# Optimization experiments

Hardware: AMD Instinct MI355X
Metric: run time of the kernel (lower is better)

The kernel has to match this reference:

```python
import jax, jax.numpy as jnp
import numpy as np

N_TAYLOR = 4

def taylor_exp_poly(x, n_terms):
    # sum_{p=0}^{n_terms-1} x^p / p!  via Horner: 1 + x*(1 + x/2*(1 + x/3*(...)))
    acc = jnp.ones_like(x)
    for p in range(n_terms - 1, 0, -1):
        acc = 1.0 + (x / p) * acc
    return acc

def setup_inputs() -> dict:
    key = jax.random.key(0)
    kq, kk, kv = jax.random.split(key, 3)
    B, H, T, d_key, d_val = 4, 8, 2048, 32, 64
    Q = jax.random.normal(kq, (B, H, T, d_key), dtype=jnp.float32)
    K = jax.random.normal(kk, (B, H, T, d_key), dtype=jnp.float32)
    V = jax.random.normal(kv, (B, H, T, d_val), dtype=jnp.float32)
    return {"Q": Q, "K": K, "V": V}

def reference(Q, K, V):
    # Symmetry-aware Taylor-approximated attention (Heinsen & Kozachkov).
    # The tightly-packed degree-p feature maps phi_p satisfy
    #   phi_p(q) . phi_p(k) == (q.k / sqrt(d_key))^p / p!
    # so summing S/Z over all n_taylor terms equals attention with kernel
    #   w(q,k) = sum_{p<n_taylor} (q.k/sqrt(d_key))^p / p!   (truncated exp),
    # causally masked and normalized by the row-sum Z.
    d_key = Q.shape[-1]
    scale = 1.0 / jnp.sqrt(jnp.asarray(d_key, dtype=Q.dtype))
    scores = jnp.einsum('bhqd,bhkd->bhqk', Q, K) * scale  # [B,H,T,T]
    A = taylor_exp_poly(scores, N_TAYLOR)
    T = Q.shape[-2]
    causal = jnp.tril(jnp.ones((T, T), dtype=bool))  # [T,T]
    A = jnp.where(causal, A, jnp.zeros((), dtype=A.dtype))
    Z = jnp.sum(A, axis=-1, keepdims=True)           # [B,H,T,1]
    S = jnp.einsum('bhqk,bhkd->bhqd', A, V)          # [B,H,T,d_val]
    return S / Z
```

## Files before the change

kernel.cpp:

```cpp
#include <hip/hip_runtime.h>
#include <hip/hip_bf16.h>


typedef __attribute__((ext_vector_type(8))) short bf16x8;
typedef __attribute__((ext_vector_type(4))) float f32x4;
typedef __attribute__((ext_vector_type(16))) float f32x16;
typedef unsigned int u32;
typedef unsigned short u16;

namespace {

constexpr int T_SEQ = 2048;
constexpr int DK    = 32;
constexpr int DV    = 64;
constexpr int NBH   = 32;

constexpr float C1 = 0.17677669529663687f;
constexpr float C2 = 0.015625f;
constexpr float C3 = 9.2071195e-4f;

constexpr size_t KHI_OFF  = 0;
constexpr size_t KLO_OFF  = (size_t)NBH * T_SEQ * DK * 2;
constexpr size_t VTHI_OFF = KLO_OFF * 2;
constexpr size_t WS_NEED  = VTHI_OFF + (size_t)NBH * DV * T_SEQ * 2;

__device__ __forceinline__ u32 pack_hi2(float f0, float f1) {
  return (__float_as_uint(f0) >> 16) | (__float_as_uint(f1) & 0xffff0000u);
}
__device__ __forceinline__ float trunc_bf(float f) {
  return __uint_as_float(__float_as_uint(f) & 0xffff0000u);
}
__device__ __forceinline__ u16 bfhi(float f) { return (u16)(__float_as_uint(f) >> 16); }

__device__ __forceinline__ u32 pack_rn2(float f0, float f1) {
  union { __hip_bfloat16 h; u16 u; } a, b;
  a.h = __hip_bfloat16(f0);
  b.h = __hip_bfloat16(f1);
  return (u32)a.u | ((u32)b.u << 16);
}

__device__ __forceinline__ void permswap(u32& a, u32& b) {
  asm volatile("v_permlane32_swap_b32 %0, %1" : "+v"(a), "+v"(b));
}


__global__ void pack_kv(const float* __restrict__ Kg, const float* __restrict__ Vg,
                        u16* __restrict__ Khi, u16* __restrict__ Klo,
                        u16* __restrict__ Vthi) {
  __shared__ float tile[DV][33];
  const int bid = blockIdx.x;
  const int t   = threadIdx.x;
  if (bid < 2048) {
    size_t i = ((size_t)bid * 256 + t) * 4;
    float4 f = *(const float4*)(Kg + i);
    ushort4 h, l;
    h.x = bfhi(f.x); h.y = bfhi(f.y); h.z = bfhi(f.z); h.w = bfhi(f.w);
    l.x = bfhi(f.x - trunc_bf(f.x)); l.y = bfhi(f.y - trunc_bf(f.y));
    l.z = bfhi(f.z - trunc_bf(f.z)); l.w = bfhi(f.w - trunc_bf(f.w));
    *(ushort4*)(Khi + i) = h;
    *(ushort4*)(Klo + i) = l;
  } else {
    const int vb = bid - 2048;
    const int bh = vb >> 6;
    const int k0 = (vb & 63) * 32;
    {
      const int kl = t >> 3, c0 = (t & 7) * 8;
      const float* src = Vg + ((size_t)bh * T_SEQ + k0 + kl) * DV + c0;
      float4 a = *(const float4*)src;
      float4 b = *(const float4*)(src + 4);
      tile[c0 + 0][kl] = a.x; tile[c0 + 1][kl] = a.y;
      tile[c0 + 2][kl] = a.z; tile[c0 + 3][kl] = a.w;
      tile[c0 + 4][kl] = b.x; tile[c0 + 5][kl] = b.y;
      tile[c0 + 6][kl] = b.z; tile[c0 + 7][kl] = b.w;
    }
    __syncthreads();
    {
      const int cl = t >> 2, k8 = (t & 3) * 8;
      u32 h[4];
#pragma unroll
      for (int j = 0; j < 4; ++j)
        h[j] = pack_rn2(tile[cl][k8 + 2 * j], tile[cl][k8 + 2 * j + 1]);
      size_t off = ((size_t)(bh * DV + cl)) * T_SEQ + k0 + k8;
      *(uint4*)(Vthi + off) = make_uint4(h[0], h[1], h[2], h[3]);
    }
  }
}


__global__ __launch_bounds__(256, 4)
void taylor_attn_v6(const float* __restrict__ Qg, const u16* __restrict__ Khi,
                    const u16* __restrict__ Klo, const u16* __restrict__ Vthi,
                    float* __restrict__ Outg) {
  __shared__ __align__(16) float Sp[4 * 2048];
  __shared__ float Zp[4 * 32];

  const int tid = threadIdx.x;
  const int l   = tid & 63;
  const int w   = tid >> 6;
  const int cq  = l & 31;
  const int hi  = l >> 5;

  const int bid = blockIdx.x;
  const int xcd = bid & 7;
  const int r_  = bid >> 3;
  const int bh  = xcd * 4 + (r_ & 3);
  const int p   = r_ >> 2;

  const u16* kbh_hi = Khi + (size_t)bh * T_SEQ * DK;
  const u16* kbh_lo = Klo + (size_t)bh * T_SEQ * DK;
  const u16* vbh_hi = Vthi + (size_t)bh * DV * T_SEQ;
  const float* qb   = Qg + (size_t)bh * T_SEQ * DK;

#pragma unroll 1
  for (int ph = 0; ph < 2; ++ph) {
    const int s  = ph ? (63 - p) : p;
    const int q0 = s * 32;

    if (ph) __syncthreads();

    bf16x8 qfh[2], qfl[2];
#pragma unroll
    for (int t = 0; t < 2; ++t) {
      const float* qp = qb + (size_t)(q0 + cq) * DK + t * 16 + hi * 8;
      float4 a = *(const float4*)qp;
      float4 b = *(const float4*)(qp + 4);
      union { bf16x8 v; u32 u[4]; } H, L;
      H.u[0] = pack_hi2(a.x, a.y); H.u[1] = pack_hi2(a.z, a.w);
      H.u[2] = pack_hi2(b.x, b.y); H.u[3] = pack_hi2(b.z, b.w);
      L.u[0] = pack_hi2(a.x - trunc_bf(a.x), a.y - trunc_bf(a.y));
      L.u[1] = pack_hi2(a.z - trunc_bf(a.z), a.w - trunc_bf(a.w));
      L.u[2] = pack_hi2(b.x - trunc_bf(b.x), b.y - trunc_bf(b.y));
      L.u[3] = pack_hi2(b.z - trunc_bf(b.z), b.w - trunc_bf(b.w));
      qfh[t] = H.v; qfl[t] = L.v;
    }

    f32x16 acc[2];
#pragma unroll
    for (int ct = 0; ct < 2; ++ct)
#pragma unroll
      for (int r = 0; r < 16; ++r) acc[ct][r] = 0.f;
    float zacc = 0.f;

    for (int kt = w; kt <= s; kt += 4) {
      const int k0 = kt * 32;

      bf16x8 kfh[2], kfl[2];
#pragma unroll
      for (int t = 0; t < 2; ++t) {
        size_t off = (size_t)(k0 + cq) * DK + t * 16 + hi * 8;
        kfh[t] = *(const bf16x8*)(kbh_hi + off);
        kfl[t] = *(const bf16x8*)(kbh_lo + off);
      }
      bf16x8 vfr[4];
#pragma unroll
      for (int ct = 0; ct < 2; ++ct)
#pragma unroll
        for (int t = 0; t < 2; ++t)
          vfr[ct * 2 + t] = *(const bf16x8*)(
              vbh_hi + (size_t)(ct * 32 + cq) * T_SEQ + k0 + t * 16 + hi * 8);

      f32x16 d0, d1;
#pragma unroll
      for (int r = 0; r < 16; ++r) { d0[r] = 0.f; d1[r] = 0.f; }
      d0 = __builtin_amdgcn_mfma_f32_32x32x16_bf16(kfh[0], qfh[0], d0, 0, 0, 0);
      d1 = __builtin_amdgcn_mfma_f32_32x32x16_bf16(kfh[1], qfh[1], d1, 0, 0, 0);
      d0 = __builtin_amdgcn_mfma_f32_32x32x16_bf16(kfh[0], qfl[0], d0, 0, 0, 0);
      d1 = __builtin_amdgcn_mfma_f32_32x32x16_bf16(kfh[1], qfl[1], d1, 0, 0, 0);
      d0 = __builtin_amdgcn_mfma_f32_32x32x16_bf16(kfl[0], qfh[0], d0, 0, 0, 0);
      d1 = __builtin_amdgcn_mfma_f32_32x32x16_bf16(kfl[1], qfh[1], d1, 0, 0, 0);

      float wv[16];
      const bool diag = (kt == s);
#pragma unroll
      for (int r = 0; r < 16; ++r) {
        float sc = d0[r] + d1[r];
        float t_ = __builtin_fmaf(sc, C3, C2);
        t_       = __builtin_fmaf(sc, t_, C1);
        float wr = __builtin_fmaf(sc, t_, 1.0f);
        if (diag) {
          const int krel = (r & 3) + 8 * (r >> 2) + 4 * hi;
          wr = (krel <= cq) ? wr : 0.f;
        }
        zacc += wr;
        wv[r] = wr;
      }

      union { bf16x8 v; u32 u[4]; } WH[2];
#pragma unroll
      for (int t = 0; t < 2; ++t) {
        const int b = t * 8;
        u32 p0 = pack_rn2(wv[b + 0], wv[b + 1]);
        u32 p1 = pack_rn2(wv[b + 2], wv[b + 3]);
        u32 p2 = pack_rn2(wv[b + 4], wv[b + 5]);
        u32 p3 = pack_rn2(wv[b + 6], wv[b + 7]);
        permswap(p0, p2); permswap(p1, p3);
        WH[t].u[0] = p0; WH[t].u[1] = p1; WH[t].u[2] = p2; WH[t].u[3] = p3;
      }

#pragma unroll
      for (int ct = 0; ct < 2; ++ct)
#pragma unroll
        for (int t = 0; t < 2; ++t)
          acc[ct] = __builtin_amdgcn_mfma_f32_32x32x16_bf16(WH[t].v, vfr[ct * 2 + t],
                                                            acc[ct], 0, 0, 0);
    }

    {
      float zt = zacc + __shfl_xor(zacc, 32);
      if (hi == 0) Zp[w * 32 + cq] = zt;
    }
#pragma unroll
    for (int ct = 0; ct < 2; ++ct)
#pragma unroll
      for (int r = 0; r < 16; ++r) {
        const int qr = (r & 3) + 8 * (r >> 2) + 4 * hi;
        Sp[w * 2048 + qr * 64 + ct * 32 + cq] = acc[ct][r];
      }
    __syncthreads();

    const f32x4* S4 = (const f32x4*)Sp;
#pragma unroll
    for (int i = 0; i < 2; ++i) {
      const int e4  = tid + i * 256;
      const int row = e4 >> 4;
      f32x4 ssum = S4[e4] + S4[512 + e4] + S4[1024 + e4] + S4[1536 + e4];
      float z = Zp[row] + Zp[32 + row] + Zp[64 + row] + Zp[96 + row];
      float inv = 1.0f / z;
      float4 o;
      o.x = ssum[0] * inv; o.y = ssum[1] * inv;
      o.z = ssum[2] * inv; o.w = ssum[3] * inv;
      *(float4*)(Outg + ((size_t)bh * T_SEQ + q0 + row) * DV + (e4 & 15) * 4) = o;
    }
  }
}


constexpr int QT_FB = 64;
constexpr int KT_FB = 32;
constexpr int LDSW  = 40;
constexpr float SCALE = 0.17677669529663687f;

__global__ __launch_bounds__(256, 4)
void taylor_attn_fb(const float* __restrict__ Qg, const float* __restrict__ Kg,
                    const float* __restrict__ Vg, float* __restrict__ Outg) {
  __shared__ __align__(16) unsigned short Qhi[QT_FB * LDSW], Qlo[QT_FB * LDSW];
  __shared__ __align__(16) unsigned short Khi_[KT_FB * LDSW], Klo_[KT_FB * LDSW];
  __shared__ __align__(16) unsigned short Vthi_[DV * LDSW], Vtlo_[DV * LDSW];
  __shared__ __align__(16) unsigned Wp[4][16 * 32];

  const int tid  = threadIdx.x;
  const int lane = tid & 63;
  const int wid  = tid >> 6;
  const int m    = lane & 15;
  const int g    = lane >> 4;

  const int bid = blockIdx.x;
  const int v   = bid >> 3;
  const int bh  = (bid & 7) * 4 + (v >> 5);
  const int qt  = 31 - (v & 31);
  const int q0  = qt * QT_FB;

  const float* Qbase = Qg + ((size_t)bh * T_SEQ + q0) * DK;
  const float* Kbase = Kg + (size_t)bh * T_SEQ * DK;
  const float* Vbase = Vg + (size_t)bh * T_SEQ * DV;

#pragma unroll
  for (int p = 0; p < 2; ++p) {
    int e = tid + p * 256, row = e >> 3, c4 = (e & 7) * 4;
    float4 f = *(const float4*)(Qbase + row * DK + c4);
    uint2 h, l;
    h.x = pack_hi2(f.x, f.y); h.y = pack_hi2(f.z, f.w);
    l.x = pack_hi2(f.x - trunc_bf(f.x), f.y - trunc_bf(f.y));
    l.y = pack_hi2(f.z - trunc_bf(f.z), f.w - trunc_bf(f.w));
    *(uint2*)&Qhi[row * LDSW + c4] = h;
    *(uint2*)&Qlo[row * LDSW + c4] = l;
  }
  __syncthreads();

  const int wq = wid * 16;
  const bf16x8 qhi = *(const bf16x8*)&Qhi[(wq + m) * LDSW + g * 8];
  const bf16x8 qlo = *(const bf16x8*)&Qlo[(wq + m) * LDSW + g * 8];

  f32x4 acc[4];
#pragma unroll
  for (int ct = 0; ct < 4; ++ct) acc[ct] = f32x4{0.f, 0.f, 0.f, 0.f};
  float zacc[4] = {0.f, 0.f, 0.f, 0.f};

  const int q_lane0 = q0 + wq + g * 4;
  const int q_wave_max = q0 + wq + 15;

  const int nkt = (q0 + QT_FB) / KT_FB;
  for (int kt = 0; kt < nkt; ++kt) {
    const int k0 = kt * KT_FB;
    __syncthreads();
    {
      int row = tid >> 3, c4 = (tid & 7) * 4;
      float4 f = *(const float4*)(Kbase + (size_t)(k0 + row) * DK + c4);
      uint2 h, l;
      h.x = pack_hi2(f.x, f.y); h.y = pack_hi2(f.z, f.w);
      l.x = pack_hi2(f.x - trunc_bf(f.x), f.y - trunc_bf(f.y));
      l.y = pack_hi2(f.z - trunc_bf(f.z), f.w - trunc_bf(f.w));
      *(uint2*)&Khi_[row * LDSW + c4] = h;
      *(uint2*)&Klo_[row * LDSW + c4] = l;
    }
    {
      int kk = (tid & 15) * 2, c4 = (tid >> 4) * 4;
      const float* vp = Vbase + (size_t)(k0 + kk) * DV + c4;
      float4 a = *(const float4*)vp;
      float4 b = *(const float4*)(vp + DV);
      float af[4] = {a.x, a.y, a.z, a.w};
      float bf_[4] = {b.x, b.y, b.z, b.w};
#pragma unroll
      for (int jj = 0; jj < 4; ++jj) {
        *(unsigned*)&Vthi_[(c4 + jj) * LDSW + kk] = pack_hi2(af[jj], bf_[jj]);
        *(unsigned*)&Vtlo_[(c4 + jj) * LDSW + kk] =
            pack_hi2(af[jj] - trunc_bf(af[jj]), bf_[jj] - trunc_bf(bf_[jj]));
      }
    }
    __syncthreads();

    if (k0 > q_wave_max) continue;

#pragma unroll
    for (int k16 = 0; k16 < 2; ++k16) {
      const int kcol0 = k16 * 16;
      bf16x8 khi = *(const bf16x8*)&Khi_[(kcol0 + m) * LDSW + g * 8];
      bf16x8 klo = *(const bf16x8*)&Klo_[(kcol0 + m) * LDSW + g * 8];
      f32x4 sc = {0.f, 0.f, 0.f, 0.f};
      sc = __builtin_amdgcn_mfma_f32_16x16x32_bf16(qhi, khi, sc, 0, 0, 0);
      sc = __builtin_amdgcn_mfma_f32_16x16x32_bf16(qhi, klo, sc, 0, 0, 0);
      sc = __builtin_amdgcn_mfma_f32_16x16x32_bf16(qlo, khi, sc, 0, 0, 0);
      const int k_abs = k0 + kcol0 + m;
      const int kcol  = kcol0 + m;
#pragma unroll
      for (int r = 0; r < 4; ++r) {
        float x  = sc[r] * SCALE;
        float a3 = __builtin_fmaf(x, 0.3333333333333333f, 1.0f);
        float a2 = __builtin_fmaf(x * 0.5f, a3, 1.0f);
        float wvv = __builtin_fmaf(x, a2, 1.0f);
        wvv = (k_abs <= q_lane0 + r) ? wvv : 0.0f;
        zacc[r] += wvv;
        float wl = wvv - trunc_bf(wvv);
        unsigned packed = (__float_as_uint(wvv) >> 16) |
                          (__float_as_uint(wl) & 0xffff0000u);
        const int q = g * 4 + r;
        Wp[wid][q * 32 + (((kcol >> 2) ^ (q & 7)) << 2) + (kcol & 3)] = packed;
      }
    }

    uint4 pa = *(const uint4*)&Wp[wid][m * 32 + (((2 * g) ^ (m & 7)) << 2)];
    uint4 pb = *(const uint4*)&Wp[wid][m * 32 + (((2 * g + 1) ^ (m & 7)) << 2)];
    union { bf16x8 v; unsigned u[4]; } WH, WL;
    WH.u[0] = (pa.x & 0xffffu) | (pa.y << 16);
    WH.u[1] = (pa.z & 0xffffu) | (pa.w << 16);
    WH.u[2] = (pb.x & 0xffffu) | (pb.y << 16);
    WH.u[3] = (pb.z & 0xffffu) | (pb.w << 16);
    WL.u[0] = (pa.x >> 16) | (pa.y & 0xffff0000u);
    WL.u[1] = (pa.z >> 16) | (pa.w & 0xffff0000u);
    WL.u[2] = (pb.x >> 16) | (pb.y & 0xffff0000u);
    WL.u[3] = (pb.z >> 16) | (pb.w & 0xffff0000u);

#pragma unroll
    for (int ct = 0; ct < 4; ++ct) {
      bf16x8 vhi = *(const bf16x8*)&Vthi_[(ct * 16 + m) * LDSW + g * 8];
      bf16x8 vlo = *(const bf16x8*)&Vtlo_[(ct * 16 + m) * LDSW + g * 8];
      acc[ct] = __builtin_amdgcn_mfma_f32_16x16x32_bf16(WH.v, vhi, acc[ct], 0, 0, 0);
      acc[ct] = __builtin_amdgcn_mfma_f32_16x16x32_bf16(WH.v, vlo, acc[ct], 0, 0, 0);
      acc[ct] = __builtin_amdgcn_mfma_f32_16x16x32_bf16(WL.v, vhi, acc[ct], 0, 0, 0);
    }
  }

  float invz[4];
#pragma unroll
  for (int r = 0; r < 4; ++r) {
    float z = zacc[r];
    z += __shfl_xor(z, 1); z += __shfl_xor(z, 2);
    z += __shfl_xor(z, 4); z += __shfl_xor(z, 8);
    invz[r] = 1.0f / z;
  }

  float* ob = Outg + ((size_t)bh * T_SEQ + (q0 + wq)) * DV;
#pragma unroll
  for (int ct = 0; ct < 4; ++ct)
#pragma unroll
    for (int r = 0; r < 4; ++r)
      ob[(g * 4 + r) * DV + ct * 16 + m] = acc[ct][r] * invz[r];
}

}

extern "C" void kernel_launch(void* const* d_in, const int* in_sizes, int n_in,
                              void* d_out, int out_size, void* d_ws, size_t ws_size,
                              hipStream_t stream) {
  const float* Q = (const float*)d_in[0];
  const float* K = (const float*)d_in[1];
  const float* V = (const float*)d_in[2];
  float* Out = (float*)d_out;

  if (ws_size >= WS_NEED && d_ws != nullptr) {
    u16* khi  = (u16*)((char*)d_ws + KHI_OFF);
    u16* klo  = (u16*)((char*)d_ws + KLO_OFF);
    u16* vthi = (u16*)((char*)d_ws + VTHI_OFF);

    hipLaunchKernelGGL(pack_kv, dim3(4096), dim3(256), 0, stream,
                       K, V, khi, klo, vthi);
    hipLaunchKernelGGL(taylor_attn_v6, dim3(1024), dim3(256), 0, stream,
                       Q, khi, klo, vthi, Out);
  } else {
    hipLaunchKernelGGL(taylor_attn_fb, dim3(1024), dim3(256), 0, stream,
                       Q, K, V, Out);
  }
}
```

Baseline: 63.08 us.

## Replace split-bf16 QK scores with single fp16 MFMA and prefetch K tiles

Drops the three-MFMA split-bf16 (hi/lo) emulation of the fp32 Q·K product and uses one fp16 MFMA pair instead. K is packed once to fp16, which halves K workspace traffic and removes the Klo buffer. The main loop is restructured: K tiles are double-buffered across iterations, and the causal diagonal tile is handled outside the loop so the mask check leaves the hot path. fp16 has 10 mantissa bits, so the scores lose some accuracy compared with the hi/lo scheme, and large inputs could overflow.

```diff
diff --git a/kernel.cpp b/kernel.cpp
--- a/kernel.cpp
+++ b/kernel.cpp
@@ -3,6 +3,7 @@
 
 
 typedef __attribute__((ext_vector_type(8))) short bf16x8;
+typedef __attribute__((ext_vector_type(8))) _Float16 f16x8;
 typedef __attribute__((ext_vector_type(4))) float f32x4;
 typedef __attribute__((ext_vector_type(16))) float f32x16;
 typedef unsigned int u32;
@@ -19,9 +20,8 @@
 constexpr float C2 = 0.015625f;
 constexpr float C3 = 9.2071195e-4f;
 
-constexpr size_t KHI_OFF  = 0;
-constexpr size_t KLO_OFF  = (size_t)NBH * T_SEQ * DK * 2;
-constexpr size_t VTHI_OFF = KLO_OFF * 2;
+constexpr size_t KHF_OFF  = 0;
+constexpr size_t VTHI_OFF = (size_t)NBH * T_SEQ * DK * 2;
 constexpr size_t WS_NEED  = VTHI_OFF + (size_t)NBH * DV * T_SEQ * 2;
 
 __device__ __forceinline__ u32 pack_hi2(float f0, float f1) {
@@ -30,35 +30,33 @@
 __device__ __forceinline__ float trunc_bf(float f) {
   return __uint_as_float(__float_as_uint(f) & 0xffff0000u);
 }
-__device__ __forceinline__ u16 bfhi(float f) { return (u16)(__float_as_uint(f) >> 16); }
-
+__device__ __forceinline__ u16 f2h(float f) {
+  union { _Float16 h; u16 u; } c;
+  c.h = (_Float16)f;
+  return c.u;
+}
 __device__ __forceinline__ u32 pack_rn2(float f0, float f1) {
   union { __hip_bfloat16 h; u16 u; } a, b;
   a.h = __hip_bfloat16(f0);
   b.h = __hip_bfloat16(f1);
   return (u32)a.u | ((u32)b.u << 16);
 }
-
 __device__ __forceinline__ void permswap(u32& a, u32& b) {
   asm volatile("v_permlane32_swap_b32 %0, %1" : "+v"(a), "+v"(b));
 }
 
 
 __global__ void pack_kv(const float* __restrict__ Kg, const float* __restrict__ Vg,
-                        u16* __restrict__ Khi, u16* __restrict__ Klo,
-                        u16* __restrict__ Vthi) {
+                        u16* __restrict__ Khf, u16* __restrict__ Vthi) {
   __shared__ float tile[DV][33];
   const int bid = blockIdx.x;
   const int t   = threadIdx.x;
   if (bid < 2048) {
     size_t i = ((size_t)bid * 256 + t) * 4;
     float4 f = *(const float4*)(Kg + i);
-    ushort4 h, l;
-    h.x = bfhi(f.x); h.y = bfhi(f.y); h.z = bfhi(f.z); h.w = bfhi(f.w);
-    l.x = bfhi(f.x - trunc_bf(f.x)); l.y = bfhi(f.y - trunc_bf(f.y));
-    l.z = bfhi(f.z - trunc_bf(f.z)); l.w = bfhi(f.w - trunc_bf(f.w));
-    *(ushort4*)(Khi + i) = h;
-    *(ushort4*)(Klo + i) = l;
+    ushort4 h;
+    h.x = f2h(f.x); h.y = f2h(f.y); h.z = f2h(f.z); h.w = f2h(f.w);
+    *(ushort4*)(Khf + i) = h;
   } else {
     const int vb = bid - 2048;
     const int bh = vb >> 6;
@@ -88,9 +86,8 @@
 
 
 __global__ __launch_bounds__(256, 4)
-void taylor_attn_v6(const float* __restrict__ Qg, const u16* __restrict__ Khi,
-                    const u16* __restrict__ Klo, const u16* __restrict__ Vthi,
-                    float* __restrict__ Outg) {
+void taylor_attn_v7(const float* __restrict__ Qg, const u16* __restrict__ Khf,
+                    const u16* __restrict__ Vthi, float* __restrict__ Outg) {
   __shared__ __align__(16) float Sp[4 * 2048];
   __shared__ float Zp[4 * 32];
 
@@ -106,10 +103,9 @@
   const int bh  = xcd * 4 + (r_ & 3);
   const int p   = r_ >> 2;
 
-  const u16* kbh_hi = Khi + (size_t)bh * T_SEQ * DK;
-  const u16* kbh_lo = Klo + (size_t)bh * T_SEQ * DK;
-  const u16* vbh_hi = Vthi + (size_t)bh * DV * T_SEQ;
-  const float* qb   = Qg + (size_t)bh * T_SEQ * DK;
+  const u16* kq = Khf + (size_t)bh * T_SEQ * DK + (size_t)cq * DK + hi * 8;
+  const u16* vq = Vthi + (size_t)bh * DV * T_SEQ + (size_t)cq * T_SEQ + hi * 8;
+  const float* qb = Qg + (size_t)bh * T_SEQ * DK;
 
 #pragma unroll 1
   for (int ph = 0; ph < 2; ++ph) {
@@ -118,62 +114,48 @@
 
     if (ph) __syncthreads();
 
-    bf16x8 qfh[2], qfl[2];
+    f16x8 qf[2];
 #pragma unroll
     for (int t = 0; t < 2; ++t) {
       const float* qp = qb + (size_t)(q0 + cq) * DK + t * 16 + hi * 8;
       float4 a = *(const float4*)qp;
       float4 b = *(const float4*)(qp + 4);
-      union { bf16x8 v; u32 u[4]; } H, L;
-      H.u[0] = pack_hi2(a.x, a.y); H.u[1] = pack_hi2(a.z, a.w);
-      H.u[2] = pack_hi2(b.x, b.y); H.u[3] = pack_hi2(b.z, b.w);
-      L.u[0] = pack_hi2(a.x - trunc_bf(a.x), a.y - trunc_bf(a.y));
-      L.u[1] = pack_hi2(a.z - trunc_bf(a.z), a.w - trunc_bf(a.w));
-      L.u[2] = pack_hi2(b.x - trunc_bf(b.x), b.y - trunc_bf(b.y));
-      L.u[3] = pack_hi2(b.z - trunc_bf(b.z), b.w - trunc_bf(b.w));
-      qfh[t] = H.v; qfl[t] = L.v;
-    }
-
-    f32x16 acc[2];
-#pragma unroll
-    for (int ct = 0; ct < 2; ++ct)
-#pragma unroll
-      for (int r = 0; r < 16; ++r) acc[ct][r] = 0.f;
+      f16x8 v;
+      v[0] = (_Float16)a.x; v[1] = (_Float16)a.y;
+      v[2] = (_Float16)a.z; v[3] = (_Float16)a.w;
+      v[4] = (_Float16)b.x; v[5] = (_Float16)b.y;
+      v[6] = (_Float16)b.z; v[7] = (_Float16)b.w;
+      qf[t] = v;
+    }
+
+    f32x16 acc0, acc1;
+#pragma unroll
+    for (int r = 0; r < 16; ++r) { acc0[r] = 0.f; acc1[r] = 0.f; }
     float zacc = 0.f;
 
-    for (int kt = w; kt <= s; kt += 4) {
-      const int k0 = kt * 32;
-
-      bf16x8 kfh[2], kfl[2];
-#pragma unroll
-      for (int t = 0; t < 2; ++t) {
-        size_t off = (size_t)(k0 + cq) * DK + t * 16 + hi * 8;
-        kfh[t] = *(const bf16x8*)(kbh_hi + off);
-        kfl[t] = *(const bf16x8*)(kbh_lo + off);
-      }
-      bf16x8 vfr[4];
+    auto LOADK = [&](f16x8* kf, int kt) {
+      const u16* kp = kq + (size_t)kt * 1024;
+      kf[0] = *(const f16x8*)kp;
+      kf[1] = *(const f16x8*)(kp + 16);
+    };
+    auto LOADV = [&](bf16x8* vf, int kt) {
 #pragma unroll
       for (int ct = 0; ct < 2; ++ct)
 #pragma unroll
         for (int t = 0; t < 2; ++t)
-          vfr[ct * 2 + t] = *(const bf16x8*)(
-              vbh_hi + (size_t)(ct * 32 + cq) * T_SEQ + k0 + t * 16 + hi * 8);
-
-      f32x16 d0, d1;
-#pragma unroll
-      for (int r = 0; r < 16; ++r) { d0[r] = 0.f; d1[r] = 0.f; }
-      d0 = __builtin_amdgcn_mfma_f32_32x32x16_bf16(kfh[0], qfh[0], d0, 0, 0, 0);
-      d1 = __builtin_amdgcn_mfma_f32_32x32x16_bf16(kfh[1], qfh[1], d1, 0, 0, 0);
-      d0 = __builtin_amdgcn_mfma_f32_32x32x16_bf16(kfh[0], qfl[0], d0, 0, 0, 0);
-      d1 = __builtin_amdgcn_mfma_f32_32x32x16_bf16(kfh[1], qfl[1], d1, 0, 0, 0);
-      d0 = __builtin_amdgcn_mfma_f32_32x32x16_bf16(kfl[0], qfh[0], d0, 0, 0, 0);
-      d1 = __builtin_amdgcn_mfma_f32_32x32x16_bf16(kfl[1], qfh[1], d1, 0, 0, 0);
-
+          vf[ct * 2 + t] = *(const bf16x8*)(
+              vq + (size_t)ct * 32 * T_SEQ + kt * 32 + t * 16);
+    };
+    auto STEP = [&](const f16x8* kf, const bf16x8* vf, bool diag) {
+      f32x16 d;
+#pragma unroll
+      for (int r = 0; r < 16; ++r) d[r] = 0.f;
+      d = __builtin_amdgcn_mfma_f32_32x32x16_f16(kf[0], qf[0], d, 0, 0, 0);
+      d = __builtin_amdgcn_mfma_f32_32x32x16_f16(kf[1], qf[1], d, 0, 0, 0);
       float wv[16];
-      const bool diag = (kt == s);
 #pragma unroll
       for (int r = 0; r < 16; ++r) {
-        float sc = d0[r] + d1[r];
+        float sc = d[r];
         float t_ = __builtin_fmaf(sc, C3, C2);
         t_       = __builtin_fmaf(sc, t_, C1);
         float wr = __builtin_fmaf(sc, t_, 1.0f);
@@ -184,7 +166,6 @@
         zacc += wr;
         wv[r] = wr;
       }
-
       union { bf16x8 v; u32 u[4]; } WH[2];
 #pragma unroll
       for (int t = 0; t < 2; ++t) {
@@ -196,13 +177,45 @@
         permswap(p0, p2); permswap(p1, p3);
         WH[t].u[0] = p0; WH[t].u[1] = p1; WH[t].u[2] = p2; WH[t].u[3] = p3;
       }
-
-#pragma unroll
-      for (int ct = 0; ct < 2; ++ct)
-#pragma unroll
-        for (int t = 0; t < 2; ++t)
-          acc[ct] = __builtin_amdgcn_mfma_f32_32x32x16_bf16(WH[t].v, vfr[ct * 2 + t],
-                                                            acc[ct], 0, 0, 0);
+      acc0 = __builtin_amdgcn_mfma_f32_32x32x16_bf16(WH[0].v, vf[0], acc0, 0, 0, 0);
+      acc0 = __builtin_amdgcn_mfma_f32_32x32x16_bf16(WH[1].v, vf[1], acc0, 0, 0, 0);
+      acc1 = __builtin_amdgcn_mfma_f32_32x32x16_bf16(WH[0].v, vf[2], acc1, 0, 0, 0);
+      acc1 = __builtin_amdgcn_mfma_f32_32x32x16_bf16(WH[1].v, vf[3], acc1, 0, 0, 0);
+    };
+
+    int kt = w;
+    f16x8 kA[2], kB[2];
+    if (kt < s) {
+      LOADK(kA, kt);
+      while (true) {
+        int kn = kt + 4;
+        if (kn < s) {
+          LOADK(kB, kn);
+          bf16x8 vf[4]; LOADV(vf, kt);
+          STEP(kA, vf, false);
+          kt = kn;
+        } else {
+          bf16x8 vf[4]; LOADV(vf, kt);
+          STEP(kA, vf, false);
+          break;
+        }
+        kn = kt + 4;
+        if (kn < s) {
+          LOADK(kA, kn);
+          bf16x8 vf[4]; LOADV(vf, kt);
+          STEP(kB, vf, false);
+          kt = kn;
+        } else {
+          bf16x8 vf[4]; LOADV(vf, kt);
+          STEP(kB, vf, false);
+          break;
+        }
+      }
+    }
+    if ((s & 3) == w) {
+      f16x8 kD[2]; LOADK(kD, s);
+      bf16x8 vf[4]; LOADV(vf, s);
+      STEP(kD, vf, true);
     }
 
     {
@@ -210,12 +223,11 @@
       if (hi == 0) Zp[w * 32 + cq] = zt;
     }
 #pragma unroll
-    for (int ct = 0; ct < 2; ++ct)
-#pragma unroll
-      for (int r = 0; r < 16; ++r) {
-        const int qr = (r & 3) + 8 * (r >> 2) + 4 * hi;
-        Sp[w * 2048 + qr * 64 + ct * 32 + cq] = acc[ct][r];
-      }
+    for (int r = 0; r < 16; ++r) {
+      const int qr = (r & 3) + 8 * (r >> 2) + 4 * hi;
+      Sp[w * 2048 + qr * 64 + cq]      = acc0[r];
+      Sp[w * 2048 + qr * 64 + 32 + cq] = acc1[r];
+    }
     __syncthreads();
 
     const f32x4* S4 = (const f32x4*)Sp;
@@ -398,14 +410,12 @@
   float* Out = (float*)d_out;
 
   if (ws_size >= WS_NEED && d_ws != nullptr) {
-    u16* khi  = (u16*)((char*)d_ws + KHI_OFF);
-    u16* klo  = (u16*)((char*)d_ws + KLO_OFF);
+    u16* khf  = (u16*)((char*)d_ws + KHF_OFF);
     u16* vthi = (u16*)((char*)d_ws + VTHI_OFF);
 
-    hipLaunchKernelGGL(pack_kv, dim3(4096), dim3(256), 0, stream,
-                       K, V, khi, klo, vthi);
-    hipLaunchKernelGGL(taylor_attn_v6, dim3(1024), dim3(256), 0, stream,
-                       Q, khi, klo, vthi, Out);
+    hipLaunchKernelGGL(pack_kv, dim3(4096), dim3(256), 0, stream, K, V, khf, vthi);
+    hipLaunchKernelGGL(taylor_attn_v7, dim3(1024), dim3(256), 0, stream,
+                       Q, khf, vthi, Out);
   } else {
     hipLaunchKernelGGL(taylor_attn_fb, dim3(1024), dim3(256), 0, stream,
                        Q, K, V, Out);
```

New measurement: 55.69 us. 1.13x faster.

## Use fp16 single-pass QK, pre-swizzled KV tiles, and LDS double-buffered staging

Applied to the files above, without the earlier changes.

Q and K are now converted to fp16 and multiplied with a single fp16 MFMA pair, replacing the three-term bf16 hi/lo split-precision product. The pack kernel writes K and V into per-tile, MFMA-fragment-ordered blocks so the attention kernel can stage them into LDS through double-buffered global_load_lds copies. Work is also redistributed: each wave owns its own 32-row query tile and the block walks the shared key tiles, which removes the cross-wave LDS reduction of S and Z at the end. The trade-offs are lower score precision from fp16 rounding, a block-wide barrier on every key tile, and lower occupancy (launch bounds changed from 4 to 2).

```diff
diff --git a/kernel.cpp b/kernel.cpp
--- a/kernel.cpp
+++ b/kernel.cpp
@@ -3,6 +3,7 @@
 
 
 typedef __attribute__((ext_vector_type(8))) short bf16x8;
+typedef __attribute__((ext_vector_type(8))) _Float16 f16x8;
 typedef __attribute__((ext_vector_type(4))) float f32x4;
 typedef __attribute__((ext_vector_type(16))) float f32x16;
 typedef unsigned int u32;
@@ -19,10 +20,8 @@
 constexpr float C2 = 0.015625f;
 constexpr float C3 = 9.2071195e-4f;
 
-constexpr size_t KHI_OFF  = 0;
-constexpr size_t KLO_OFF  = (size_t)NBH * T_SEQ * DK * 2;
-constexpr size_t VTHI_OFF = KLO_OFF * 2;
-constexpr size_t WS_NEED  = VTHI_OFF + (size_t)NBH * DV * T_SEQ * 2;
+constexpr int    TILE_U16 = 3072;
+constexpr size_t WS_NEED  = (size_t)NBH * 64 * TILE_U16 * 2;
 
 __device__ __forceinline__ u32 pack_hi2(float f0, float f1) {
   return (__float_as_uint(f0) >> 16) | (__float_as_uint(f1) & 0xffff0000u);
@@ -30,69 +29,61 @@
 __device__ __forceinline__ float trunc_bf(float f) {
   return __uint_as_float(__float_as_uint(f) & 0xffff0000u);
 }
-__device__ __forceinline__ u16 bfhi(float f) { return (u16)(__float_as_uint(f) >> 16); }
-
+__device__ __forceinline__ u16 f2h(float f) {
+  union { _Float16 h; u16 u; } c;
+  c.h = (_Float16)f;
+  return c.u;
+}
+__device__ __forceinline__ u16 bfr(float f) {
+  union { __hip_bfloat16 h; u16 u; } c;
+  c.h = __hip_bfloat16(f);
+  return c.u;
+}
 __device__ __forceinline__ u32 pack_rn2(float f0, float f1) {
-  union { __hip_bfloat16 h; u16 u; } a, b;
-  a.h = __hip_bfloat16(f0);
-  b.h = __hip_bfloat16(f1);
-  return (u32)a.u | ((u32)b.u << 16);
-}
-
+  return (u32)bfr(f0) | ((u32)bfr(f1) << 16);
+}
 __device__ __forceinline__ void permswap(u32& a, u32& b) {
   asm volatile("v_permlane32_swap_b32 %0, %1" : "+v"(a), "+v"(b));
 }
-
-
-__global__ void pack_kv(const float* __restrict__ Kg, const float* __restrict__ Vg,
-                        u16* __restrict__ Khi, u16* __restrict__ Klo,
-                        u16* __restrict__ Vthi) {
-  __shared__ float tile[DV][33];
+__device__ __forceinline__ void load16_lds(const u16* g, u16* lp) {
+  __builtin_amdgcn_global_load_lds(
+      (const __attribute__((address_space(1))) u32*)(const void*)g,
+      (__attribute__((address_space(3))) u32*)(void*)lp, 16, 0, 0);
+}
+
+__global__ void pack_kv9(const float* __restrict__ Kg, const float* __restrict__ Vg,
+                         u16* __restrict__ P) {
   const int bid = blockIdx.x;
-  const int t   = threadIdx.x;
-  if (bid < 2048) {
-    size_t i = ((size_t)bid * 256 + t) * 4;
-    float4 f = *(const float4*)(Kg + i);
-    ushort4 h, l;
-    h.x = bfhi(f.x); h.y = bfhi(f.y); h.z = bfhi(f.z); h.w = bfhi(f.w);
-    l.x = bfhi(f.x - trunc_bf(f.x)); l.y = bfhi(f.y - trunc_bf(f.y));
-    l.z = bfhi(f.z - trunc_bf(f.z)); l.w = bfhi(f.w - trunc_bf(f.w));
-    *(ushort4*)(Khi + i) = h;
-    *(ushort4*)(Klo + i) = l;
-  } else {
-    const int vb = bid - 2048;
-    const int bh = vb >> 6;
-    const int k0 = (vb & 63) * 32;
-    {
-      const int kl = t >> 3, c0 = (t & 7) * 8;
-      const float* src = Vg + ((size_t)bh * T_SEQ + k0 + kl) * DV + c0;
-      float4 a = *(const float4*)src;
-      float4 b = *(const float4*)(src + 4);
-      tile[c0 + 0][kl] = a.x; tile[c0 + 1][kl] = a.y;
-      tile[c0 + 2][kl] = a.z; tile[c0 + 3][kl] = a.w;
-      tile[c0 + 4][kl] = b.x; tile[c0 + 5][kl] = b.y;
-      tile[c0 + 6][kl] = b.z; tile[c0 + 7][kl] = b.w;
-    }
-    __syncthreads();
-    {
-      const int cl = t >> 2, k8 = (t & 3) * 8;
-      u32 h[4];
-#pragma unroll
-      for (int j = 0; j < 4; ++j)
-        h[j] = pack_rn2(tile[cl][k8 + 2 * j], tile[cl][k8 + 2 * j + 1]);
-      size_t off = ((size_t)(bh * DV + cl)) * T_SEQ + k0 + k8;
-      *(uint4*)(Vthi + off) = make_uint4(h[0], h[1], h[2], h[3]);
-    }
-  }
-}
-
-
-__global__ __launch_bounds__(256, 4)
-void taylor_attn_v6(const float* __restrict__ Qg, const u16* __restrict__ Khi,
-                    const u16* __restrict__ Klo, const u16* __restrict__ Vthi,
+  const int bh = bid >> 6, kt = bid & 63;
+  const int k0 = kt * 32;
+  u16* tile = P + (size_t)bid * TILE_U16;
+  for (int g = threadIdx.x; g < 384; g += 256) {
+    const int seg = g >> 6;
+    const int l = g & 63, lo = l & 31, hi = l >> 5;
+    ushort4 o0, o1;
+    if (seg < 2) {
+      const float* src = Kg + ((size_t)bh * T_SEQ + k0 + lo) * DK + seg * 16 + hi * 8;
+      o0.x = f2h(src[0]); o0.y = f2h(src[1]); o0.z = f2h(src[2]); o0.w = f2h(src[3]);
+      o1.x = f2h(src[4]); o1.y = f2h(src[5]); o1.z = f2h(src[6]); o1.w = f2h(src[7]);
+    } else {
+      const int ct = (seg - 2) >> 1, t = (seg - 2) & 1;
+      const float* src = Vg + ((size_t)bh * T_SEQ + k0 + t * 16 + hi * 8) * DV
+                         + ct * 32 + lo;
+      o0.x = bfr(src[0 * DV]); o0.y = bfr(src[1 * DV]);
+      o0.z = bfr(src[2 * DV]); o0.w = bfr(src[3 * DV]);
+      o1.x = bfr(src[4 * DV]); o1.y = bfr(src[5 * DV]);
+      o1.z = bfr(src[6 * DV]); o1.w = bfr(src[7 * DV]);
+    }
+    *(ushort4*)(tile + g * 8)     = o0;
+    *(ushort4*)(tile + g * 8 + 4) = o1;
+  }
+}
+
+
+__global__ __launch_bounds__(256, 2)
+void taylor_attn_v9(const float* __restrict__ Qg, const u16* __restrict__ P,
                     float* __restrict__ Outg) {
-  __shared__ __align__(16) float Sp[4 * 2048];
-  __shared__ float Zp[4 * 32];
+  __shared__ __align__(16) u16 KV[2][TILE_U16];
 
   const int tid = threadIdx.x;
   const int l   = tid & 63;
@@ -100,80 +91,67 @@
   const int cq  = l & 31;
   const int hi  = l >> 5;
 
-  const int bid = blockIdx.x;
-  const int xcd = bid & 7;
-  const int r_  = bid >> 3;
-  const int bh  = xcd * 4 + (r_ & 3);
-  const int p   = r_ >> 2;
-
-  const u16* kbh_hi = Khi + (size_t)bh * T_SEQ * DK;
-  const u16* kbh_lo = Klo + (size_t)bh * T_SEQ * DK;
-  const u16* vbh_hi = Vthi + (size_t)bh * DV * T_SEQ;
-  const float* qb   = Qg + (size_t)bh * T_SEQ * DK;
+  const int bid  = blockIdx.x;
+  const int bh   = bid >> 4;
+  const int e    = bid & 15;
+  const int core = (e >> 1) & 7;
+  const int a    = (e & 1) ? (15 - core) : core;
+  const int sw   = 4 * a + w;
+  const int q0w  = sw * 32;
+  const int klast = 4 * a + 3;
+
+  const u16* tb = P + (size_t)bh * 64 * TILE_U16;
+
+  f16x8 qf0, qf1;
+  {
+    const float* qp = Qg + ((size_t)bh * T_SEQ + q0w + cq) * DK + hi * 8;
+    float4 a0 = *(const float4*)qp;
+    float4 a1 = *(const float4*)(qp + 4);
+    float4 b0 = *(const float4*)(qp + 16);
+    float4 b1 = *(const float4*)(qp + 20);
+    qf0[0] = (_Float16)a0.x; qf0[1] = (_Float16)a0.y;
+    qf0[2] = (_Float16)a0.z; qf0[3] = (_Float16)a0.w;
+    qf0[4] = (_Float16)a1.x; qf0[5] = (_Float16)a1.y;
+    qf0[6] = (_Float16)a1.z; qf0[7] = (_Float16)a1.w;
+    qf1[0] = (_Float16)b0.x; qf1[1] = (_Float16)b0.y;
+    qf1[2] = (_Float16)b0.z; qf1[3] = (_Float16)b0.w;
+    qf1[4] = (_Float16)b1.x; qf1[5] = (_Float16)b1.y;
+    qf1[6] = (_Float16)b1.z; qf1[7] = (_Float16)b1.w;
+  }
+
+  f32x16 ZERO;
+#pragma unroll
+  for (int r = 0; r < 16; ++r) ZERO[r] = 0.f;
+  f32x16 acc0 = ZERO, acc1 = ZERO;
+  float zacc = 0.f;
+
+  auto STAGE = [&](int buf, int kt) {
+    const u16* g = tb + (size_t)kt * TILE_U16;
+    load16_lds(g + w * 512 + l * 8, &KV[buf][w * 512]);
+    if (w < 2)
+      load16_lds(g + (w + 4) * 512 + l * 8, &KV[buf][(w + 4) * 512]);
+  };
+
+  STAGE(0, 0);
+  __syncthreads();
+  int cur = 0;
 
 #pragma unroll 1
-  for (int ph = 0; ph < 2; ++ph) {
-    const int s  = ph ? (63 - p) : p;
-    const int q0 = s * 32;
-
-    if (ph) __syncthreads();
-
-    bf16x8 qfh[2], qfl[2];
-#pragma unroll
-    for (int t = 0; t < 2; ++t) {
-      const float* qp = qb + (size_t)(q0 + cq) * DK + t * 16 + hi * 8;
-      float4 a = *(const float4*)qp;
-      float4 b = *(const float4*)(qp + 4);
-      union { bf16x8 v; u32 u[4]; } H, L;
-      H.u[0] = pack_hi2(a.x, a.y); H.u[1] = pack_hi2(a.z, a.w);
-      H.u[2] = pack_hi2(b.x, b.y); H.u[3] = pack_hi2(b.z, b.w);
-      L.u[0] = pack_hi2(a.x - trunc_bf(a.x), a.y - trunc_bf(a.y));
-      L.u[1] = pack_hi2(a.z - trunc_bf(a.z), a.w - trunc_bf(a.w));
-      L.u[2] = pack_hi2(b.x - trunc_bf(b.x), b.y - trunc_bf(b.y));
-      L.u[3] = pack_hi2(b.z - trunc_bf(b.z), b.w - trunc_bf(b.w));
-      qfh[t] = H.v; qfl[t] = L.v;
-    }
-
-    f32x16 acc[2];
-#pragma unroll
-    for (int ct = 0; ct < 2; ++ct)
-#pragma unroll
-      for (int r = 0; r < 16; ++r) acc[ct][r] = 0.f;
-    float zacc = 0.f;
-
-    for (int kt = w; kt <= s; kt += 4) {
-      const int k0 = kt * 32;
-
-      bf16x8 kfh[2], kfl[2];
-#pragma unroll
-      for (int t = 0; t < 2; ++t) {
-        size_t off = (size_t)(k0 + cq) * DK + t * 16 + hi * 8;
-        kfh[t] = *(const bf16x8*)(kbh_hi + off);
-        kfl[t] = *(const bf16x8*)(kbh_lo + off);
-      }
-      bf16x8 vfr[4];
-#pragma unroll
-      for (int ct = 0; ct < 2; ++ct)
-#pragma unroll
-        for (int t = 0; t < 2; ++t)
-          vfr[ct * 2 + t] = *(const bf16x8*)(
-              vbh_hi + (size_t)(ct * 32 + cq) * T_SEQ + k0 + t * 16 + hi * 8);
-
-      f32x16 d0, d1;
-#pragma unroll
-      for (int r = 0; r < 16; ++r) { d0[r] = 0.f; d1[r] = 0.f; }
-      d0 = __builtin_amdgcn_mfma_f32_32x32x16_bf16(kfh[0], qfh[0], d0, 0, 0, 0);
-      d1 = __builtin_amdgcn_mfma_f32_32x32x16_bf16(kfh[1], qfh[1], d1, 0, 0, 0);
-      d0 = __builtin_amdgcn_mfma_f32_32x32x16_bf16(kfh[0], qfl[0], d0, 0, 0, 0);
-      d1 = __builtin_amdgcn_mfma_f32_32x32x16_bf16(kfh[1], qfl[1], d1, 0, 0, 0);
-      d0 = __builtin_amdgcn_mfma_f32_32x32x16_bf16(kfl[0], qfh[0], d0, 0, 0, 0);
-      d1 = __builtin_amdgcn_mfma_f32_32x32x16_bf16(kfl[1], qfh[1], d1, 0, 0, 0);
+  for (int kt = 0; kt <= klast; ++kt) {
+    if (kt < klast) STAGE(cur ^ 1, kt + 1);
+
+    if (kt <= sw) {
+      const u16* B = &KV[cur][0];
+      f16x8 kf0 = *(const f16x8*)(B + l * 8);
+      f16x8 kf1 = *(const f16x8*)(B + 512 + l * 8);
+      f32x16 d = __builtin_amdgcn_mfma_f32_32x32x16_f16(kf0, qf0, ZERO, 0, 0, 0);
+      d = __builtin_amdgcn_mfma_f32_32x32x16_f16(kf1, qf1, d, 0, 0, 0);
 
       float wv[16];
-      const bool diag = (kt == s);
+      const bool diag = (kt == sw);
 #pragma unroll
       for (int r = 0; r < 16; ++r) {
-        float sc = d0[r] + d1[r];
+        float sc = d[r];
         float t_ = __builtin_fmaf(sc, C3, C2);
         t_       = __builtin_fmaf(sc, t_, C1);
         float wr = __builtin_fmaf(sc, t_, 1.0f);
@@ -197,40 +175,30 @@
         WH[t].u[0] = p0; WH[t].u[1] = p1; WH[t].u[2] = p2; WH[t].u[3] = p3;
       }
 
-#pragma unroll
-      for (int ct = 0; ct < 2; ++ct)
-#pragma unroll
-        for (int t = 0; t < 2; ++t)
-          acc[ct] = __builtin_amdgcn_mfma_f32_32x32x16_bf16(WH[t].v, vfr[ct * 2 + t],
-                                                            acc[ct], 0, 0, 0);
-    }
-
-    {
-      float zt = zacc + __shfl_xor(zacc, 32);
-      if (hi == 0) Zp[w * 32 + cq] = zt;
-    }
-#pragma unroll
-    for (int ct = 0; ct < 2; ++ct)
-#pragma unroll
-      for (int r = 0; r < 16; ++r) {
-        const int qr = (r & 3) + 8 * (r >> 2) + 4 * hi;
-        Sp[w * 2048 + qr * 64 + ct * 32 + cq] = acc[ct][r];
-      }
+      bf16x8 v00 = *(const bf16x8*)(B + 1024 + l * 8);
+      bf16x8 v01 = *(const bf16x8*)(B + 1536 + l * 8);
+      bf16x8 v10 = *(const bf16x8*)(B + 2048 + l * 8);
+      bf16x8 v11 = *(const bf16x8*)(B + 2560 + l * 8);
+      acc0 = __builtin_amdgcn_mfma_f32_32x32x16_bf16(WH[0].v, v00, acc0, 0, 0, 0);
+      acc0 = __builtin_amdgcn_mfma_f32_32x32x16_bf16(WH[1].v, v01, acc0, 0, 0, 0);
+      acc1 = __builtin_amdgcn_mfma_f32_32x32x16_bf16(WH[0].v, v10, acc1, 0, 0, 0);
+      acc1 = __builtin_amdgcn_mfma_f32_32x32x16_bf16(WH[1].v, v11, acc1, 0, 0, 0);
+    }
+
     __syncthreads();
-
-    const f32x4* S4 = (const f32x4*)Sp;
-#pragma unroll
-    for (int i = 0; i < 2; ++i) {
-      const int e4  = tid + i * 256;
-      const int row = e4 >> 4;
-      f32x4 ssum = S4[e4] + S4[512 + e4] + S4[1024 + e4] + S4[1536 + e4];
-      float z = Zp[row] + Zp[32 + row] + Zp[64 + row] + Zp[96 + row];
-      float inv = 1.0f / z;
-      float4 o;
-      o.x = ssum[0] * inv; o.y = ssum[1] * inv;
-      o.z = ssum[2] * inv; o.w = ssum[3] * inv;
-      *(float4*)(Outg + ((size_t)bh * T_SEQ + q0 + row) * DV + (e4 & 15) * 4) = o;
-    }
+    cur ^= 1;
+  }
+
+  float zt = zacc + __shfl_xor(zacc, 32);
+  float iz = 1.0f / zt;
+
+  float* ob = Outg + ((size_t)bh * T_SEQ + q0w) * DV;
+#pragma unroll
+  for (int r = 0; r < 16; ++r) {
+    const int qr = (r & 3) + 8 * (r >> 2) + 4 * hi;
+    float izr = __shfl(iz, qr);
+    ob[(size_t)qr * DV + cq]      = acc0[r] * izr;
+    ob[(size_t)qr * DV + 32 + cq] = acc1[r] * izr;
   }
 }
 
@@ -398,14 +366,10 @@
   float* Out = (float*)d_out;
 
   if (ws_size >= WS_NEED && d_ws != nullptr) {
-    u16* khi  = (u16*)((char*)d_ws + KHI_OFF);
-    u16* klo  = (u16*)((char*)d_ws + KLO_OFF);
-    u16* vthi = (u16*)((char*)d_ws + VTHI_OFF);
-
-    hipLaunchKernelGGL(pack_kv, dim3(4096), dim3(256), 0, stream,
-                       K, V, khi, klo, vthi);
-    hipLaunchKernelGGL(taylor_attn_v6, dim3(1024), dim3(256), 0, stream,
-                       Q, khi, klo, vthi, Out);
+    u16* P = (u16*)d_ws;
+    hipLaunchKernelGGL(pack_kv9, dim3(2048), dim3(256), 0, stream, K, V, P);
+    hipLaunchKernelGGL(taylor_attn_v9, dim3(512), dim3(256), 0, stream,
+                       Q, P, Out);
   } else {
     hipLaunchKernelGGL(taylor_attn_fb, dim3(1024), dim3(256), 0, stream,
                        Q, K, V, Out);
```

Result: faster. 58.25 us (-7.6%).
